# Kernel tuning notes

Hardware: AMD Instinct MI355X
Metric: run time of the kernel (lower is better)

The kernel has to match this reference:

```python
import jax, jax.numpy as jnp
import numpy as np
import math
from functools import lru_cache

# ---------- Clebsch-Gordan machinery (numpy, setup-time only) ----------

def _cg(j1, m1, j2, m2, j, m):
    """Complex-basis CG coefficient via Racah's formula (Condon-Shortley)."""
    if m1 + m2 != m:
        return 0.0
    f = math.factorial
    pre = (2 * j + 1) * f(j1 + j2 - j) * f(j1 - j2 + j) * f(-j1 + j2 + j) / f(j1 + j2 + j + 1)
    pre *= f(j1 + m1) * f(j1 - m1) * f(j2 + m2) * f(j2 - m2) * f(j + m) * f(j - m)
    s = 0.0
    for k in range(0, j1 + j2 - j + 1):
        d = (k, j1 + j2 - j - k, j1 - m1 - k, j2 + m2 - k, j - j2 + m1 + k, j - j1 - m2 + k)
        if min(d) < 0:
            continue
        s += (-1) ** k / (f(d[0]) * f(d[1]) * f(d[2]) * f(d[3]) * f(d[4]) * f(d[5]))
    return math.sqrt(pre) * s


def _csh_to_rsh(j):
    """Unitary complex->real spherical harmonics transform, columns indexed by real m."""
    C = np.zeros((2 * j + 1, 2 * j + 1), dtype=np.complex128)
    s2 = 1.0 / math.sqrt(2.0)
    for m in range(-j, j + 1):
        am = abs(m)
        if m < 0:
            C[j + m, j + m] = 1j * s2
            C[j - m, j + m] = -1j * ((-1) ** am) * s2
        elif m == 0:
            C[j, j] = 1.0
        else:
            C[j - m, j + m] = s2
            C[j + m, j + m] = ((-1) ** am) * s2
    return C


@lru_cache(maxsize=None)
def _rsh_cg(j1, j2, j):
    """Real-basis CG, compactified to rows [m1, m2, m, coeff] over nonzeros."""
    csh = np.zeros((2 * j1 + 1, 2 * j2 + 1, 2 * j + 1), dtype=np.complex128)
    for m1 in range(-j1, j1 + 1):
        for m2 in range(-j2, j2 + 1):
            m = m1 + m2
            if -j <= m <= j:
                csh[j1 + m1, j2 + m2, j + m] = _cg(j1, m1, j2, m2, j, m)
    r = np.einsum('abc,ai,bj,ck->ijk', csh, _csh_to_rsh(j1), _csh_to_rsh(j2), np.conj(_csh_to_rsh(j)))
    r = np.real(r * ((-1j) ** (j1 + j2 + j)))
    m1g, m2g, mg = np.meshgrid(np.arange(-j1, j1 + 1), np.arange(-j2, j2 + 1),
                               np.arange(-j, j + 1), indexing='ij')
    mask = np.abs(r) > 1e-12
    return np.stack([m1g[mask].astype(np.float64), m2g[mask].astype(np.float64),
                     mg[mask].astype(np.float64), r[mask]], axis=0)


def _build_coupler(md1, md2, trunc_in=True):
    """Faithful replay of CGPCoupler._init_params: returns cg_tilde, repids, out_dim."""
    md1 = np.asarray(md1, dtype=np.int64)
    md2 = np.asarray(md2, dtype=np.int64)
    md_in = np.stack([md1, md2], axis=0)                      # [2, 2*(L+1)]
    max_n_out = np.maximum(md1, md2)
    nlp = md_in.shape[1]
    n_irr = np.repeat(np.arange(nlp // 2) * 2 + 1, 2)         # irreps per (l,p) slot
    off_in = np.cumsum(md_in * n_irr[None, :], axis=1)
    off_in = np.concatenate([np.zeros((2, 1), dtype=np.int64), off_in[:, :-1]], axis=1)
    max_l = nlp // 2 - 1
    md_out = np.zeros_like(max_n_out)
    valid = []
    for lout in range(max_l + 1):
        for pout in (1, -1):
            for l1 in range(max_l + 1):
                for l2 in range(max_l + 1):
                    for p1 in (1, -1):
                        for p2 in (1, -1):
                            cp = (-1) ** (lout + l1 + l2)
                            if p1 * p2 * cp != pout:
                                continue
                            if l1 + l2 < lout or abs(l1 - l2) > lout:
                                continue
                            lp1 = 2 * l1 + (1 - p1) // 2
                            lp2 = 2 * l2 + (1 - p2) // 2
                            lpo = 2 * lout + (1 - pout) // 2
                            if trunc_in:
                                if l1 + l2 > max_l:
                                    continue
                                deg = min(md_in[0, lp1], md_in[1, lp2],
                                          max_n_out[2 * (l1 + l2) + (1 - pout) // 2])
                            else:
                                deg = min(md_in[0, lp1], md_in[1, lp2], max_n_out[lpo])
                            md_out[lpo] += deg
                            if deg > 0:
                                valid.append((lpo, lp1, lp2, int(deg)))
    off_out = np.cumsum(md_out * n_irr)
    off_out = np.concatenate([[0], off_out[:-1]]).astype(np.int64)
    cg_l, r1_l, r2_l, ro_l = [], [], [], []
    ns_off, lpo_last = 0, 0
    for lpo, lp1, lp2, deg in valid:
        if lpo > lpo_last:
            ns_off = 0
        l1, l2, lout = lp1 // 2, lp2 // 2, lpo // 2
        src = _rsh_cg(l1, l2, lout)                            # [4, nnz]
        seg = np.repeat(src, deg, axis=1)                      # repeat_interleave along dim=1
        ns = np.tile(np.arange(deg, dtype=np.int64), src.shape[1])
        r1_l.append(off_in[0, lp1] + np.rint(seg[0] + l1).astype(np.int64) * md_in[0, lp1] + ns)
        r2_l.append(off_in[1, lp2] + np.rint(seg[1] + l2).astype(np.int64) * md_in[1, lp2] + ns)
        ro_l.append(off_out[lpo] + np.rint(seg[2] + lout).astype(np.int64) * md_out[lpo] + ns_off + ns)
        cg_l.append(seg[3])
        ns_off += deg
        lpo_last = lpo
    out_dim = int(np.sum(md_out * n_irr))
    return (np.concatenate(cg_l), np.concatenate(r1_l), np.concatenate(r2_l),
            np.concatenate(ro_l), out_dim)


METADATA = [32, 32, 32, 32, 32, 32, 32, 32]   # max_l = 3, 32 channels per (l, parity)
BATCH = 2048


def setup_inputs() -> dict:
    key = jax.random.key(0)
    k1, k2 = jax.random.split(key)
    cg, r1, r2, ro, out_dim = _build_coupler(METADATA, METADATA, trunc_in=True)
    n_irr = np.repeat(np.arange(len(METADATA) // 2) * 2 + 1, 2)
    in_dim = int(np.sum(np.asarray(METADATA) * n_irr))        # 1024
    x1 = jax.random.normal(k1, (BATCH, in_dim), dtype=jnp.float32)
    x2 = jax.random.normal(k2, (BATCH, in_dim), dtype=jnp.float32)
    return {
        "x1": x1,
        "x2": x2,
        "cg_tilde": jnp.asarray(cg, dtype=jnp.float32),
        "repids_in1": jnp.asarray(r1, dtype=jnp.int64) if jax.config.jax_enable_x64 else jnp.asarray(r1, dtype=jnp.int32),
        "repids_in2": jnp.asarray(r2, dtype=jnp.int64) if jax.config.jax_enable_x64 else jnp.asarray(r2, dtype=jnp.int32),
        "repids_out": jnp.asarray(ro, dtype=jnp.int64) if jax.config.jax_enable_x64 else jnp.asarray(ro, dtype=jnp.int32),
        "out_dim": out_dim,
    }


def reference(x1, x2, cg_tilde, repids_in1, repids_in2, repids_out, out_dim):
    # gather along rep dim (last), elementwise multiply with CG coeffs, scatter-add
    out_tilde = x1[:, repids_in1] * x2[:, repids_in2] * cg_tilde[None, :]   # [B, K]
    out = jnp.zeros((x1.shape[0], out_dim), dtype=x1.dtype).at[:, repids_out].add(out_tilde)
    return out
```

## Files before the change

### kernel.cpp

```cpp
#include <hip/hip_runtime.h>


#define IN_DIM  1024
#define ROWS    4
#define NOBCAP  512
#define SKIP_OB 511u

__global__ __launch_bounds__(1024) void prep_kernel(
    const int* __restrict__ r1, const int* __restrict__ r2,
    const int* __restrict__ ro, const float* __restrict__ cg,
    int nseg, int nob,
    uint2* __restrict__ qdesc, uint2* __restrict__ ddesc, uint2* __restrict__ sdesc,
    int* __restrict__ zlist, int* __restrict__ hdr)
{
    __shared__ int cntS[NOBCAP], rankS[NOBCAP];
    __shared__ int qoffS[NOBCAP], doffS[NOBCAP], soffS[NOBCAP];
    __shared__ unsigned long long wsumS[8], woffS[8];
    const int t = threadIdx.x;

    if (t < NOBCAP) { cntS[t] = 0; rankS[t] = 0; }
    __syncthreads();

    for (int s = t; s < nseg; s += 1024)
        atomicAdd(&cntS[ro[s << 5] >> 5], 1);
    __syncthreads();

    int c = 0;
    unsigned long long pv = 0ull;
    if (t < NOBCAP) {
        c = (t < nob) ? cntS[t] : 0;
        unsigned long long q = 0, df = 0, sf = 0, zf = 0;
        if (t < nob) {
            if (c == 2)      df = 1;
            else if (c <= 1) sf = 1;
            else { q = (unsigned long long)((c + 3) >> 2); if (c > 4) zf = 1; }
        }
        pv = (q << 48) | (df << 32) | (sf << 16) | zf;
    }
    const int lane = t & 63;
    const int wid  = t >> 6;
    #pragma unroll
    for (int off = 1; off < 64; off <<= 1) {
        const unsigned long long n = __shfl_up(pv, off, 64);
        if (lane >= off) pv += n;
    }
    if (t < NOBCAP && lane == 63) wsumS[wid] = pv;
    __syncthreads();
    if (t < 8) {
        unsigned long long v = wsumS[t];
        const unsigned long long self = v;
        #pragma unroll
        for (int off = 1; off < 8; off <<= 1) {
            const unsigned long long n = __shfl_up(v, off, 64);
            if (t >= off) v += n;
        }
        woffS[t] = v - self;
    }
    __syncthreads();

    if (t < NOBCAP) {
        const unsigned long long incl = pv + woffS[wid];
        const int qi = (int)(incl >> 48);
        const int di = (int)((incl >> 32) & 0xFFFFull);
        const int si = (int)((incl >> 16) & 0xFFFFull);
        const int zi = (int)(incl & 0xFFFFull);
        if (t < nob) {
            if (c == 2) {
                doffS[t] = di - 1;
            } else if (c <= 1) {
                soffS[t] = si - 1;
                if (c == 0)
                    sdesc[si - 1] = make_uint2(((unsigned int)t << 20) | 0x80000000u, 0u);
            } else {
                const int qn = (c + 3) >> 2;
                const int qb = qi - qn;
                qoffS[t] = qb;
                const unsigned int fl = (c > 4) ? 0u : 0x80000000u;
                if (c > 4) zlist[zi - 1] = t;
                const unsigned int pd = ((unsigned int)t << 20) | fl;
                for (int j = (qb << 2) + c; j < ((qb + qn) << 2); ++j)
                    qdesc[j] = make_uint2(pd, 0u);
            }
        }
        if (t == NOBCAP - 1) {
            const int nq = qi, nd = di, ns = si;
            const int nqPad = (nq + 15) & ~15;
            const int ndPad = (nd + 31) & ~31;
            const int nsPad = (ns + 63) & ~63;
            const uint2 dummy = make_uint2(SKIP_OB << 20, 0u);
            for (int j = (nq << 2); j < (nqPad << 2); ++j) qdesc[j] = dummy;
            for (int j = (nd << 1); j < (ndPad << 1); ++j) ddesc[j] = dummy;
            for (int j = ns;        j < nsPad;        ++j) sdesc[j] = dummy;
            hdr[0] = nqPad; hdr[1] = zi; hdr[2] = ndPad; hdr[3] = nsPad;
        }
    }
    __syncthreads();

    for (int s = t; s < nseg; s += 1024) {
        const int k  = s << 5;
        const int ob = ro[k] >> 5;
        const int cc = cntS[ob];
        const int rk = atomicAdd(&rankS[ob], 1);
        const unsigned int fl = (cc > 4) ? 0u : 0x80000000u;
        const uint2 v = make_uint2((unsigned int)r1[k] | ((unsigned int)r2[k] << 10)
                                   | ((unsigned int)ob << 20) | fl,
                                   __float_as_uint(cg[k]));
        if (cc == 2)      ddesc[(doffS[ob] << 1) + rk] = v;
        else if (cc == 1) sdesc[soffS[ob]] = v;
        else              qdesc[(qoffS[ob] << 2) + rk] = v;
    }
}

__device__ __forceinline__ void accum4(float4& acc, unsigned int dx, unsigned int dc,
                                       const float* xs1, const float* xs2)
{
    const float  c = __uint_as_float(dc);
    const float4 u = *reinterpret_cast<const float4*>(xs1 + (dx & 1023u));
    const float4 v = *reinterpret_cast<const float4*>(xs2 + ((dx >> 10) & 1023u));
    acc.x = fmaf(c, u.x * v.x, acc.x);
    acc.y = fmaf(c, u.y * v.y, acc.y);
    acc.z = fmaf(c, u.z * v.z, acc.z);
    acc.w = fmaf(c, u.w * v.w, acc.w);
}

__device__ __forceinline__ void terminal(float* orow, unsigned int hx, float4 acc)
{
    const int ob = (int)((hx >> 20) & 511u);
    if (ob == (int)SKIP_OB) return;
    float* p = orow + (ob << 5);
    if (hx >> 31) {
        *reinterpret_cast<float4*>(p) = acc;
    } else {
        unsafeAtomicAdd(p,     acc.x);
        unsafeAtomicAdd(p + 1, acc.y);
        unsafeAtomicAdd(p + 2, acc.z);
        unsafeAtomicAdd(p + 3, acc.w);
    }
}

__global__ __launch_bounds__(512) void cgp_main(const float* __restrict__ x1,
    const float* __restrict__ x2, const uint2* __restrict__ qdesc,
    const uint2* __restrict__ ddesc, const uint2* __restrict__ sdesc,
    const int* __restrict__ zlist, const int* __restrict__ hdr,
    float* __restrict__ out, int out_dim)
{
    __shared__ float x1s[ROWS * IN_DIM];
    __shared__ float x2s[ROWS * IN_DIM];
    const int r0  = blockIdx.x * ROWS;
    const int tid = threadIdx.x;

    {
        const float4* p1 = reinterpret_cast<const float4*>(x1 + (size_t)r0 * IN_DIM);
        const float4* p2 = reinterpret_cast<const float4*>(x2 + (size_t)r0 * IN_DIM);
        float4* s1 = reinterpret_cast<float4*>(x1s);
        float4* s2 = reinterpret_cast<float4*>(x2s);
        #pragma unroll
        for (int j = tid; j < (ROWS * IN_DIM) >> 2; j += 512) { s1[j] = p1[j]; s2[j] = p2[j]; }
    }
    const int nz = hdr[1];
    for (int i = tid; i < (nz << 5); i += 512) {
        const int ob = zlist[i >> 5];
        const int ch = i & 31;
        float* p = out + (size_t)r0 * out_dim + (ob << 5) + ch;
        #pragma unroll
        for (int j = 0; j < ROWS; ++j) p[j * out_dim] = 0.f;
    }
    __syncthreads();

    const int w  = tid >> 6;
    const int ln = tid & 63;
    const bool hi = (ln >> 5) != 0;
    const int hl = ln & 31;
    const int rr = hl >> 3;
    const int tt = hl & 7;
    const float* xs1 = x1s + rr * IN_DIM + (tt << 2);
    const float* xs2 = x2s + rr * IN_DIM + (tt << 2);
    float* orow = out + (size_t)(r0 + rr) * out_dim + (tt << 2);

    {
        const int qpw = hdr[0] >> 3;
        const uint2* qd = qdesc + ((size_t)(w * qpw) << 2);
        for (int i = 0; i < qpw; i += 2, qd += 8) {
            const uint4 A0 = *reinterpret_cast<const uint4*>(qd);
            const uint4 B0 = *reinterpret_cast<const uint4*>(qd + 2);
            const uint4 A1 = *reinterpret_cast<const uint4*>(qd + 4);
            const uint4 B1 = *reinterpret_cast<const uint4*>(qd + 6);
            const uint4 A  = hi ? A1 : A0;
            const uint4 Bq = hi ? B1 : B0;
            float4 acc = make_float4(0.f, 0.f, 0.f, 0.f);
            accum4(acc, A.x,  A.y,  xs1, xs2);
            accum4(acc, A.z,  A.w,  xs1, xs2);
            accum4(acc, Bq.x, Bq.y, xs1, xs2);
            accum4(acc, Bq.z, Bq.w, xs1, xs2);
            terminal(orow, A.x, acc);
        }
    }

    {
        const int dpw = hdr[2] >> 3;
        const uint2* dd = ddesc + ((size_t)(w * dpw) << 1);
        for (int i = 0; i < dpw; i += 4, dd += 8) {
            const uint4 A0 = *reinterpret_cast<const uint4*>(dd);
            const uint4 B0 = *reinterpret_cast<const uint4*>(dd + 2);
            const uint4 A1 = *reinterpret_cast<const uint4*>(dd + 4);
            const uint4 B1 = *reinterpret_cast<const uint4*>(dd + 6);
            const uint4 A  = hi ? A1 : A0;
            const uint4 Bq = hi ? B1 : B0;
            float4 a0 = make_float4(0.f, 0.f, 0.f, 0.f);
            float4 a1 = make_float4(0.f, 0.f, 0.f, 0.f);
            accum4(a0, A.x,  A.y,  xs1, xs2);
            accum4(a0, A.z,  A.w,  xs1, xs2);
            accum4(a1, Bq.x, Bq.y, xs1, xs2);
            accum4(a1, Bq.z, Bq.w, xs1, xs2);
            terminal(orow, A.x,  a0);
            terminal(orow, Bq.x, a1);
        }
    }

    {
        const int spw = hdr[3] >> 3;
        const uint2* sd = sdesc + (size_t)(w * spw);
        for (int i = 0; i < spw; i += 8, sd += 8) {
            const uint4 A0 = *reinterpret_cast<const uint4*>(sd);
            const uint4 B0 = *reinterpret_cast<const uint4*>(sd + 2);
            const uint4 A1 = *reinterpret_cast<const uint4*>(sd + 4);
            const uint4 B1 = *reinterpret_cast<const uint4*>(sd + 6);
            const uint4 A  = hi ? A1 : A0;
            const uint4 Bq = hi ? B1 : B0;
            float4 a0 = make_float4(0.f, 0.f, 0.f, 0.f);
            float4 a1 = make_float4(0.f, 0.f, 0.f, 0.f);
            float4 a2 = make_float4(0.f, 0.f, 0.f, 0.f);
            float4 a3 = make_float4(0.f, 0.f, 0.f, 0.f);
            accum4(a0, A.x,  A.y,  xs1, xs2);
            accum4(a1, A.z,  A.w,  xs1, xs2);
            accum4(a2, Bq.x, Bq.y, xs1, xs2);
            accum4(a3, Bq.z, Bq.w, xs1, xs2);
            terminal(orow, A.x,  a0);
            terminal(orow, A.z,  a1);
            terminal(orow, Bq.x, a2);
            terminal(orow, Bq.z, a3);
        }
    }
}

extern "C" void kernel_launch(void* const* d_in, const int* in_sizes, int n_in,
                              void* d_out, int out_size, void* d_ws, size_t ws_size,
                              hipStream_t stream)
{
    const float* x1 = (const float*)d_in[0];
    const float* x2 = (const float*)d_in[1];
    const float* cg = (const float*)d_in[2];
    const int*   r1 = (const int*)d_in[3];
    const int*   r2 = (const int*)d_in[4];
    const int*   ro = (const int*)d_in[5];
    float* out = (float*)d_out;

    const int B       = in_sizes[0] / IN_DIM;
    const int out_dim = out_size / B;
    const int K       = in_sizes[2];
    const int nseg    = K >> 5;
    const int nob     = out_dim >> 5;
    const int qcap    = nob + (nseg >> 2) + 32;
    const int dcap    = nob + 48;
    const int scap    = nob + 80;

    auto align16 = [](size_t v) { return (v + 15) & ~(size_t)15; };
    char* ws = (char*)d_ws;
    uint2* qdesc = (uint2*)ws;  ws += align16((size_t)qcap * 4 * sizeof(uint2));
    uint2* ddesc = (uint2*)ws;  ws += align16((size_t)dcap * 2 * sizeof(uint2));
    uint2* sdesc = (uint2*)ws;  ws += align16((size_t)scap * sizeof(uint2));
    int*   zlist = (int*)ws;    ws += align16((size_t)NOBCAP * sizeof(int));
    int*   hdr   = (int*)ws;

    hipLaunchKernelGGL(prep_kernel, dim3(1), dim3(1024), 0, stream,
                       r1, r2, ro, cg, nseg, nob, qdesc, ddesc, sdesc, zlist, hdr);
    hipLaunchKernelGGL(cgp_main, dim3(B / ROWS), dim3(512), 0, stream,
                       x1, x2, qdesc, ddesc, sdesc, zlist, hdr, out, out_dim);
}
```

Measured before the change: 29.74 us.

## Fuse descriptor-building prep kernel into main kernel with per-block shared descriptors

```diff
diff --git a/kernel.cpp b/kernel.cpp
--- a/kernel.cpp
+++ b/kernel.cpp
@@ -5,30 +5,75 @@
 #define ROWS    4
 #define NOBCAP  512
 #define SKIP_OB 511u
-
-__global__ __launch_bounds__(1024) void prep_kernel(
+#define QSLOTS  1024
+#define DSLOTS  640
+#define SSLOTS  384
+
+__device__ __forceinline__ void accum4(float4& acc, unsigned int dx, unsigned int dc,
+                                       const float* xs1, const float* xs2)
+{
+    const float  c = __uint_as_float(dc);
+    const float4 u = *reinterpret_cast<const float4*>(xs1 + (dx & 1023u));
+    const float4 v = *reinterpret_cast<const float4*>(xs2 + ((dx >> 10) & 1023u));
+    acc.x = fmaf(c, u.x * v.x, acc.x);
+    acc.y = fmaf(c, u.y * v.y, acc.y);
+    acc.z = fmaf(c, u.z * v.z, acc.z);
+    acc.w = fmaf(c, u.w * v.w, acc.w);
+}
+
+__device__ __forceinline__ void terminal(float* orow, unsigned int hx, float4 acc)
+{
+    const int ob = (int)((hx >> 20) & 511u);
+    if (ob == (int)SKIP_OB) return;
+    float* p = orow + (ob << 5);
+    if (hx >> 31) {
+        *reinterpret_cast<float4*>(p) = acc;
+    } else {
+        unsafeAtomicAdd(p,     acc.x);
+        unsafeAtomicAdd(p + 1, acc.y);
+        unsafeAtomicAdd(p + 2, acc.z);
+        unsafeAtomicAdd(p + 3, acc.w);
+    }
+}
+
+__global__ __launch_bounds__(512) void cgp_fused(
+    const float* __restrict__ x1, const float* __restrict__ x2,
     const int* __restrict__ r1, const int* __restrict__ r2,
     const int* __restrict__ ro, const float* __restrict__ cg,
-    int nseg, int nob,
-    uint2* __restrict__ qdesc, uint2* __restrict__ ddesc, uint2* __restrict__ sdesc,
-    int* __restrict__ zlist, int* __restrict__ hdr)
-{
+    int nseg, int nob, float* __restrict__ out, int out_dim)
+{
+    __shared__ float x1s[ROWS * IN_DIM];
+    __shared__ float x2s[ROWS * IN_DIM];
+    __shared__ uint2 qdescL[QSLOTS];
+    __shared__ uint2 ddescL[DSLOTS];
+    __shared__ uint2 sdescL[SSLOTS];
     __shared__ int cntS[NOBCAP], rankS[NOBCAP];
     __shared__ int qoffS[NOBCAP], doffS[NOBCAP], soffS[NOBCAP];
     __shared__ unsigned long long wsumS[8], woffS[8];
-    const int t = threadIdx.x;
-
-    if (t < NOBCAP) { cntS[t] = 0; rankS[t] = 0; }
-    __syncthreads();
-
-    for (int s = t; s < nseg; s += 1024)
+    __shared__ int zlistL[128];
+    __shared__ int hdrL[4];
+
+    const int r0  = blockIdx.x * ROWS;
+    const int t   = threadIdx.x;
+
+    {
+        const float4* p1 = reinterpret_cast<const float4*>(x1 + (size_t)r0 * IN_DIM);
+        const float4* p2 = reinterpret_cast<const float4*>(x2 + (size_t)r0 * IN_DIM);
+        float4* s1 = reinterpret_cast<float4*>(x1s);
+        float4* s2 = reinterpret_cast<float4*>(x2s);
+        #pragma unroll
+        for (int j = t; j < (ROWS * IN_DIM) >> 2; j += 512) { s1[j] = p1[j]; s2[j] = p2[j]; }
+    }
+
+    cntS[t] = 0; rankS[t] = 0;
+    __syncthreads();
+    for (int s = t; s < nseg; s += 512)
         atomicAdd(&cntS[ro[s << 5] >> 5], 1);
     __syncthreads();
 
-    int c = 0;
-    unsigned long long pv = 0ull;
-    if (t < NOBCAP) {
-        c = (t < nob) ? cntS[t] : 0;
+    const int c = (t < nob) ? cntS[t] : 0;
+    unsigned long long pv;
+    {
         unsigned long long q = 0, df = 0, sf = 0, zf = 0;
         if (t < nob) {
             if (c == 2)      df = 1;
@@ -44,7 +89,7 @@
         const unsigned long long n = __shfl_up(pv, off, 64);
         if (lane >= off) pv += n;
     }
-    if (t < NOBCAP && lane == 63) wsumS[wid] = pv;
+    if (lane == 63) wsumS[wid] = pv;
     __syncthreads();
     if (t < 8) {
         unsigned long long v = wsumS[t];
@@ -58,7 +103,7 @@
     }
     __syncthreads();
 
-    if (t < NOBCAP) {
+    {
         const unsigned long long incl = pv + woffS[wid];
         const int qi = (int)(incl >> 48);
         const int di = (int)((incl >> 32) & 0xFFFFull);
@@ -70,16 +115,16 @@
             } else if (c <= 1) {
                 soffS[t] = si - 1;
                 if (c == 0)
-                    sdesc[si - 1] = make_uint2(((unsigned int)t << 20) | 0x80000000u, 0u);
+                    sdescL[si - 1] = make_uint2(((unsigned int)t << 20) | 0x80000000u, 0u);
             } else {
                 const int qn = (c + 3) >> 2;
                 const int qb = qi - qn;
                 qoffS[t] = qb;
                 const unsigned int fl = (c > 4) ? 0u : 0x80000000u;
-                if (c > 4) zlist[zi - 1] = t;
+                if (c > 4) zlistL[zi - 1] = t;
                 const unsigned int pd = ((unsigned int)t << 20) | fl;
                 for (int j = (qb << 2) + c; j < ((qb + qn) << 2); ++j)
-                    qdesc[j] = make_uint2(pd, 0u);
+                    qdescL[j] = make_uint2(pd, 0u);
             }
         }
         if (t == NOBCAP - 1) {
@@ -88,15 +133,15 @@
             const int ndPad = (nd + 31) & ~31;
             const int nsPad = (ns + 63) & ~63;
             const uint2 dummy = make_uint2(SKIP_OB << 20, 0u);
-            for (int j = (nq << 2); j < (nqPad << 2); ++j) qdesc[j] = dummy;
-            for (int j = (nd << 1); j < (ndPad << 1); ++j) ddesc[j] = dummy;
-            for (int j = ns;        j < nsPad;        ++j) sdesc[j] = dummy;
-            hdr[0] = nqPad; hdr[1] = zi; hdr[2] = ndPad; hdr[3] = nsPad;
-        }
-    }
-    __syncthreads();
-
-    for (int s = t; s < nseg; s += 1024) {
+            for (int j = (nq << 2); j < (nqPad << 2); ++j) qdescL[j] = dummy;
+            for (int j = (nd << 1); j < (ndPad << 1); ++j) ddescL[j] = dummy;
+            for (int j = ns;        j < nsPad;        ++j) sdescL[j] = dummy;
+            hdrL[0] = nqPad; hdrL[1] = zi; hdrL[2] = ndPad; hdrL[3] = nsPad;
+        }
+    }
+    __syncthreads();
+
+    for (int s = t; s < nseg; s += 512) {
         const int k  = s << 5;
         const int ob = ro[k] >> 5;
         const int cc = cntS[ob];
@@ -105,61 +150,15 @@
         const uint2 v = make_uint2((unsigned int)r1[k] | ((unsigned int)r2[k] << 10)
                                    | ((unsigned int)ob << 20) | fl,
                                    __float_as_uint(cg[k]));
-        if (cc == 2)      ddesc[(doffS[ob] << 1) + rk] = v;
-        else if (cc == 1) sdesc[soffS[ob]] = v;
-        else              qdesc[(qoffS[ob] << 2) + rk] = v;
-    }
-}
-
-__device__ __forceinline__ void accum4(float4& acc, unsigned int dx, unsigned int dc,
-                                       const float* xs1, const float* xs2)
-{
-    const float  c = __uint_as_float(dc);
-    const float4 u = *reinterpret_cast<const float4*>(xs1 + (dx & 1023u));
-    const float4 v = *reinterpret_cast<const float4*>(xs2 + ((dx >> 10) & 1023u));
-    acc.x = fmaf(c, u.x * v.x, acc.x);
-    acc.y = fmaf(c, u.y * v.y, acc.y);
-    acc.z = fmaf(c, u.z * v.z, acc.z);
-    acc.w = fmaf(c, u.w * v.w, acc.w);
-}
-
-__device__ __forceinline__ void terminal(float* orow, unsigned int hx, float4 acc)
-{
-    const int ob = (int)((hx >> 20) & 511u);
-    if (ob == (int)SKIP_OB) return;
-    float* p = orow + (ob << 5);
-    if (hx >> 31) {
-        *reinterpret_cast<float4*>(p) = acc;
-    } else {
-        unsafeAtomicAdd(p,     acc.x);
-        unsafeAtomicAdd(p + 1, acc.y);
-        unsafeAtomicAdd(p + 2, acc.z);
-        unsafeAtomicAdd(p + 3, acc.w);
-    }
-}
-
-__global__ __launch_bounds__(512) void cgp_main(const float* __restrict__ x1,
-    const float* __restrict__ x2, const uint2* __restrict__ qdesc,
-    const uint2* __restrict__ ddesc, const uint2* __restrict__ sdesc,
-    const int* __restrict__ zlist, const int* __restrict__ hdr,
-    float* __restrict__ out, int out_dim)
-{
-    __shared__ float x1s[ROWS * IN_DIM];
-    __shared__ float x2s[ROWS * IN_DIM];
-    const int r0  = blockIdx.x * ROWS;
-    const int tid = threadIdx.x;
-
-    {
-        const float4* p1 = reinterpret_cast<const float4*>(x1 + (size_t)r0 * IN_DIM);
-        const float4* p2 = reinterpret_cast<const float4*>(x2 + (size_t)r0 * IN_DIM);
-        float4* s1 = reinterpret_cast<float4*>(x1s);
-        float4* s2 = reinterpret_cast<float4*>(x2s);
-        #pragma unroll
-        for (int j = tid; j < (ROWS * IN_DIM) >> 2; j += 512) { s1[j] = p1[j]; s2[j] = p2[j]; }
-    }
-    const int nz = hdr[1];
-    for (int i = tid; i < (nz << 5); i += 512) {
-        const int ob = zlist[i >> 5];
+        if (cc == 2)      ddescL[(doffS[ob] << 1) + rk] = v;
+        else if (cc == 1) sdescL[soffS[ob]] = v;
+        else              qdescL[(qoffS[ob] << 2) + rk] = v;
+    }
+    __syncthreads();
+
+    const int nz = hdrL[1];
+    for (int i = t; i < (nz << 5); i += 512) {
+        const int ob = zlistL[i >> 5];
         const int ch = i & 31;
         float* p = out + (size_t)r0 * out_dim + (ob << 5) + ch;
         #pragma unroll
@@ -167,8 +166,8 @@
     }
     __syncthreads();
 
-    const int w  = tid >> 6;
-    const int ln = tid & 63;
+    const int w  = t >> 6;
+    const int ln = t & 63;
     const bool hi = (ln >> 5) != 0;
     const int hl = ln & 31;
     const int rr = hl >> 3;
@@ -178,8 +177,8 @@
     float* orow = out + (size_t)(r0 + rr) * out_dim + (tt << 2);
 
     {
-        const int qpw = hdr[0] >> 3;
-        const uint2* qd = qdesc + ((size_t)(w * qpw) << 2);
+        const int qpw = hdrL[0] >> 3;
+        const uint2* qd = qdescL + ((size_t)(w * qpw) << 2);
         for (int i = 0; i < qpw; i += 2, qd += 8) {
             const uint4 A0 = *reinterpret_cast<const uint4*>(qd);
             const uint4 B0 = *reinterpret_cast<const uint4*>(qd + 2);
@@ -195,10 +194,9 @@
             terminal(orow, A.x, acc);
         }
     }
-
-    {
-        const int dpw = hdr[2] >> 3;
-        const uint2* dd = ddesc + ((size_t)(w * dpw) << 1);
+    {
+        const int dpw = hdrL[2] >> 3;
+        const uint2* dd = ddescL + ((size_t)(w * dpw) << 1);
         for (int i = 0; i < dpw; i += 4, dd += 8) {
             const uint4 A0 = *reinterpret_cast<const uint4*>(dd);
             const uint4 B0 = *reinterpret_cast<const uint4*>(dd + 2);
@@ -216,10 +214,9 @@
             terminal(orow, Bq.x, a1);
         }
     }
-
-    {
-        const int spw = hdr[3] >> 3;
-        const uint2* sd = sdesc + (size_t)(w * spw);
+    {
+        const int spw = hdrL[3] >> 3;
+        const uint2* sd = sdescL + (size_t)(w * spw);
         for (int i = 0; i < spw; i += 8, sd += 8) {
             const uint4 A0 = *reinterpret_cast<const uint4*>(sd);
             const uint4 B0 = *reinterpret_cast<const uint4*>(sd + 2);
@@ -260,20 +257,7 @@
     const int K       = in_sizes[2];
     const int nseg    = K >> 5;
     const int nob     = out_dim >> 5;
-    const int qcap    = nob + (nseg >> 2) + 32;
-    const int dcap    = nob + 48;
-    const int scap    = nob + 80;
-
-    auto align16 = [](size_t v) { return (v + 15) & ~(size_t)15; };
-    char* ws = (char*)d_ws;
-    uint2* qdesc = (uint2*)ws;  ws += align16((size_t)qcap * 4 * sizeof(uint2));
-    uint2* ddesc = (uint2*)ws;  ws += align16((size_t)dcap * 2 * sizeof(uint2));
-    uint2* sdesc = (uint2*)ws;  ws += align16((size_t)scap * sizeof(uint2));
-    int*   zlist = (int*)ws;    ws += align16((size_t)NOBCAP * sizeof(int));
-    int*   hdr   = (int*)ws;
-
-    hipLaunchKernelGGL(prep_kernel, dim3(1), dim3(1024), 0, stream,
-                       r1, r2, ro, cg, nseg, nob, qdesc, ddesc, sdesc, zlist, hdr);
-    hipLaunchKernelGGL(cgp_main, dim3(B / ROWS), dim3(512), 0, stream,
-                       x1, x2, qdesc, ddesc, sdesc, zlist, hdr, out, out_dim);
-}
+
+    hipLaunchKernelGGL(cgp_fused, dim3(B / ROWS), dim3(512), 0, stream,
+                       x1, x2, r1, r2, ro, cg, nseg, nob, out, out_dim);
+}
```

After: 29.50 us. No clear change (-0.8%).
